# Performance work log

Hardware: AMD Instinct MI355X
Metric: run time of the kernel (lower is better)

Reference implementation:

```python
import jax, jax.numpy as jnp
import numpy as np

N_NODES = 32767   # complete binary tree, depth 15
EMB_DIM = 256
HIDDEN = 256      # 'hidden_size' -> LSTM state is 2*HIDDEN
VOCAB = 32        # len(ExprNode.TYPE_LIST)


def setup_inputs() -> dict:
    key = jax.random.key(0)
    k1, k2, k3, k4, k5, k6 = jax.random.split(key, 6)
    H2 = 2 * HIDDEN
    types = jax.random.randint(k1, (N_NODES,), 0, VOCAB, dtype=jnp.int32)
    # complete binary tree: children of node i are 2i+1 / 2i+2; sentinel slot N = zero state
    idx = np.arange(N_NODES)
    a = 2 * idx + 1
    b = 2 * idx + 2
    a = np.where(a < N_NODES, a, N_NODES).astype(np.int32)
    b = np.where(b < N_NODES, b, N_NODES).astype(np.int32)
    scale = 1.0 / np.sqrt(H2)
    return {
        "types": types,
        "a_idx": jnp.asarray(a),
        "b_idx": jnp.asarray(b),
        "emb": jax.random.normal(k2, (VOCAB, EMB_DIM), jnp.float32) * 0.02,
        "W_ih": jax.random.normal(k3, (4 * H2, EMB_DIM), jnp.float32) * scale,
        "W_hh": jax.random.normal(k4, (4 * H2, H2), jnp.float32) * scale,
        "b_ih": jax.random.normal(k5, (4 * H2,), jnp.float32) * scale,
        "b_hh": jax.random.normal(k6, (4 * H2,), jnp.float32) * scale,
    }


def reference(types, a_idx, b_idx, emb, W_ih, W_hh, b_ih, b_hh):
    """Recursive binary tree-LSTM over topological (leaves-first) order.
    Each node's LSTM state has size 2H; a parent's incoming (h, c) is the concat
    of the first H entries of each child's state (zeros for missing children).
    Returns per-node hidden outputs [N, 2H] (the out_map, indexed by node id)."""
    N = types.shape[0]
    H2 = W_hh.shape[1]
    H = H2 // 2
    # batched input projection for all nodes at once: [N, 4*H2]
    x_proj = emb[types] @ W_ih.T + (b_ih + b_hh)
    Hs0 = jnp.zeros((N + 1, H2), x_proj.dtype)  # slot N = h0 (zeros)
    Cs0 = jnp.zeros((N + 1, H2), x_proj.dtype)
    order = jnp.arange(N - 1, -1, -1)  # children (higher index) before parents

    def step(carry, i):
        Hs, Cs = carry
        h = jnp.concatenate([Hs[a_idx[i], :H], Hs[b_idx[i], :H]])  # [2H]
        c = jnp.concatenate([Cs[a_idx[i], :H], Cs[b_idx[i], :H]])
        gates = x_proj[i] + W_hh @ h                 # [4*H2], torch gate order i,f,g,o
        ig, fg, gg, og = jnp.split(gates, 4)
        c_new = jax.nn.sigmoid(fg) * c + jax.nn.sigmoid(ig) * jnp.tanh(gg)
        h_new = jax.nn.sigmoid(og) * jnp.tanh(c_new)
        return (Hs.at[i].set(h_new), Cs.at[i].set(c_new)), h_new

    _, outs = jax.lax.scan(step, (Hs0, Cs0), order)
    return outs[::-1]  # reorder so row i is node i's output
```

## Files before the change

kernel.cpp:

```cpp
#include <hip/hip_runtime.h>
#include <hip/hip_bf16.h>


#define NNODES 32767

typedef __attribute__((ext_vector_type(8))) short bf16x8;
typedef __attribute__((ext_vector_type(4))) float f32x4;

typedef const __attribute__((address_space(1))) void* gptr_t;
typedef __attribute__((address_space(3))) void* lptr_t;

__device__ __forceinline__ float sigf(float x) { return 1.0f / (1.0f + __expf(-x)); }
__device__ __forceinline__ float tanhfast(float x) { return 2.0f / (1.0f + __expf(-2.0f * x)) - 1.0f; }

__device__ __forceinline__ short bf_hi(float x) {
    __hip_bfloat16 h = __float2bfloat16(x);
    return __builtin_bit_cast(short, h);
}
__device__ __forceinline__ float bf_f(short s) {
    __hip_bfloat16 h = __builtin_bit_cast(__hip_bfloat16, s);
    return __bfloat162float(h);
}
__device__ __forceinline__ void split8(const float* src, short* hi, short* lo) {
#pragma unroll
    for (int j = 0; j < 8; ++j) {
        float x = src[j];
        short h = bf_hi(x);
        hi[j] = h;
        lo[j] = bf_hi(x - bf_f(h));
    }
}

__global__ void proj_kernel(const float* __restrict__ emb, const float* __restrict__ W_ih,
                            const float* __restrict__ b_ih, const float* __restrict__ b_hh,
                            float* __restrict__ proj) {
    __shared__ float e[256];
    int v = blockIdx.x >> 3;
    int rc = blockIdx.x & 7;
    int t = threadIdx.x;
    e[t] = emb[v * 256 + t];
    __syncthreads();
    int r = rc * 256 + t;
    const float4* w4 = (const float4*)(W_ih + (size_t)r * 256);
    const float4* e4 = (const float4*)e;
    float acc = 0.f;
#pragma unroll 8
    for (int k = 0; k < 64; ++k) {
        float4 w = w4[k];
        float4 h = e4[k];
        acc += w.x * h.x + w.y * h.y + w.z * h.z + w.w * h.w;
    }
    proj[v * 2048 + r] = acc + b_ih[r] + b_hh[r];
}

__global__ void wpack_kernel(const float* __restrict__ W_hh,
                             short* __restrict__ Whi, short* __restrict__ Wlo) {
    int t = blockIdx.x * 256 + threadIdx.x;
    int lane = t & 63;
    int kt = (t >> 6) & 15;
    int ntile = t >> 10;
    int n = ntile * 16 + (lane & 15);
    int k0 = kt * 32 + (lane >> 4) * 8;
    const float* src = W_hh + (size_t)n * 512 + k0;
    short hi[8], lo[8];
    split8(src, hi, lo);
    *(bf16x8*)(Whi + (size_t)t * 8) = *(bf16x8*)hi;
    *(bf16x8*)(Wlo + (size_t)t * 8) = *(bf16x8*)lo;
}

__global__ void leaf_kernel(const int* __restrict__ types, const float* __restrict__ proj,
                            float* __restrict__ out, float* __restrict__ C256,
                            short* __restrict__ Hsplit) {
    int bi = blockIdx.x;
    int node = 16383 + (bi >> 1);
    int j = ((bi & 1) << 8) + threadIdx.x;
    int tt = types[node];
    const float* p = proj + (size_t)tt * 2048;
    float gi = p[j];
    float gg = p[1024 + j];
    float go = p[1536 + j];
    float cn = sigf(gi) * tanhfast(gg);
    float hn = sigf(go) * tanhfast(cn);
    out[(size_t)node * 512 + j] = hn;
    if ((bi & 1) == 0) {
        C256[(size_t)node * 256 + j] = cn;
        short hi = bf_hi(hn);
        Hsplit[(size_t)node * 512 + j] = hi;
        Hsplit[(size_t)node * 512 + 256 + j] = bf_hi(hn - bf_f(hi));
    }
}

__global__ __launch_bounds__(256) void big_gemm_lstm_kernel(
    const int* __restrict__ a_idx, const int* __restrict__ b_idx,
    const int* __restrict__ types, float* __restrict__ out,
    const float* __restrict__ proj, float* __restrict__ C256,
    short* __restrict__ Hsplit, int node_base) {
    __shared__ __align__(16) short lds[2][16384];
    __shared__ int sA[128], sB[128], sT[128];

    const unsigned WOFF = 16777216u;

    int t = threadIdx.x;
    int lin = blockIdx.x;
    int x = lin >> 4;
    int y = (lin & 7) * 2 + ((lin >> 3) & 1);
    int node0 = node_base + x * 128;
    int j0 = y * 32;

    if (t < 128) {
        sA[t] = a_idx[node0 + t];
        sB[t] = b_idx[node0 + t];
        sT[t] = types[node0 + t];
    }
    __syncthreads();

    int w = t >> 6, lane = t & 63;
    int wm = w >> 1, wn = w & 1;

    unsigned b0[8], b1[8], sk;
    if (w < 2) {
        sk = 32u;
#pragma unroll
        for (int i = 0; i < 8; ++i) {
            int ca = w * 8 + i;
            int rl = lane >> 3;
            int r_loc = ca * 8 + rl;
            int j = (lane & 7) ^ rl;
            unsigned ks = (unsigned)(j >> 2) * 256u + (unsigned)(j & 3) * 8u;
            b0[i] = (unsigned)sA[r_loc] * 512u + ks;
            b1[i] = (unsigned)sB[r_loc] * 512u + ks;
        }
    } else {
        sk = 512u;
#pragma unroll
        for (int i = 0; i < 8; ++i) {
            int cc = (w - 2) * 8 + i;
            int nt = cc >> 1, part = cc & 1;
            int q = nt >> 1, sub = nt & 1;
            unsigned ntg = (unsigned)(q * 32 + y * 2 + sub);
            b0[i] = WOFF + ntg * 8192u + (unsigned)part * 1048576u + (unsigned)lane * 8u;
            b1[i] = b0[i] + 4096u;
        }
    }

    f32x4 acc[4][4];
#pragma unroll
    for (int i = 0; i < 4; ++i)
#pragma unroll
        for (int q = 0; q < 4; ++q) acc[i][q] = (f32x4){0.f, 0.f, 0.f, 0.f};

    auto stage = [&](int kt, int buf) {
#pragma unroll
        for (int i = 0; i < 8; ++i) {
            unsigned off = ((kt < 8) ? b0[i] : b1[i]) + (unsigned)(kt & 7) * sk;
            const short* gsrc = Hsplit + off;
            short* ldst = &lds[buf][(w * 8 + i) * 512];
            __builtin_amdgcn_global_load_lds((gptr_t)gsrc, (lptr_t)ldst, 16, 0, 0);
        }
    };

    auto compute = [&](int buf) {
        const short* L = lds[buf];
        int s = lane >> 4;
        bf16x8 ah[4], al[4];
#pragma unroll
        for (int i = 0; i < 4; ++i) {
            int m_loc = (wm * 4 + i) * 16 + (lane & 15);
            int ch = m_loc >> 3;
            int r = m_loc & 7;
            const short* base = L + ch * 512 + r * 64;
            ah[i] = *(const bf16x8*)&base[(s ^ r) * 8];
            al[i] = *(const bf16x8*)&base[((4 + s) ^ r) * 8];
        }
        __builtin_amdgcn_s_setprio(1);
#pragma unroll
        for (int q = 0; q < 4; ++q) {
            int nt = q * 2 + wn;
            bf16x8 bh = *(const bf16x8*)&L[(16 + nt * 2) * 512 + lane * 8];
            bf16x8 bl = *(const bf16x8*)&L[(17 + nt * 2) * 512 + lane * 8];
#pragma unroll
            for (int i = 0; i < 4; ++i) {
                acc[i][q] = __builtin_amdgcn_mfma_f32_16x16x32_bf16(ah[i], bh, acc[i][q], 0, 0, 0);
                acc[i][q] = __builtin_amdgcn_mfma_f32_16x16x32_bf16(ah[i], bl, acc[i][q], 0, 0, 0);
                acc[i][q] = __builtin_amdgcn_mfma_f32_16x16x32_bf16(al[i], bh, acc[i][q], 0, 0, 0);
            }
        }
        __builtin_amdgcn_s_setprio(0);
    };

    stage(0, 0);
    int cur = 0;
#pragma unroll 1
    for (int kt = 0; kt < 16; ++kt) {
        __builtin_amdgcn_s_barrier();
        if (kt < 15) stage(kt + 1, cur ^ 1);
        if (kt < 15) {
            asm volatile("s_waitcnt vmcnt(8)" ::: "memory");
        } else {
            asm volatile("s_waitcnt vmcnt(0)" ::: "memory");
        }
        __builtin_amdgcn_s_barrier();
        compute(cur);
        cur ^= 1;
    }

    int j = j0 + wn * 16 + (lane & 15);
    bool fh = (j < 256);
    int jc = j & 255;
#pragma unroll
    for (int i = 0; i < 4; ++i) {
        int mrow = wm * 64 + i * 16 + (lane >> 4) * 4;
#pragma unroll
        for (int r = 0; r < 4; ++r) {
            int m_loc = mrow + r;
            int node = node0 + m_loc;
            const float* p = proj + (size_t)sT[m_loc] * 2048 + j;
            float gi = acc[i][0][r] + p[0];
            float gf = acc[i][1][r] + p[512];
            float gg = acc[i][2][r] + p[1024];
            float go = acc[i][3][r] + p[1536];
            int child = fh ? sA[m_loc] : sB[m_loc];
            float c = C256[(size_t)child * 256 + jc];
            float cn = sigf(gf) * c + sigf(gi) * tanhfast(gg);
            float hn = sigf(go) * tanhfast(cn);
            out[(size_t)node * 512 + j] = hn;
            if (fh) {
                C256[(size_t)node * 256 + j] = cn;
                short hi = bf_hi(hn);
                Hsplit[(size_t)node * 512 + j] = hi;
                Hsplit[(size_t)node * 512 + 256 + j] = bf_hi(hn - bf_f(hi));
            }
        }
    }
}

__global__ __launch_bounds__(256) void gemm_lstm_kernel(
    const int* __restrict__ a_idx, const int* __restrict__ b_idx,
    const int* __restrict__ types, float* __restrict__ out,
    const short* __restrict__ Whi, const short* __restrict__ Wlo,
    const float* __restrict__ proj, float* __restrict__ C256,
    short* __restrict__ Hsplit, int node_base, int Jc) {
    __shared__ short Ahi[2][16][64][8];
    __shared__ short Alo[2][16][64][8];
    __shared__ int sA[32], sB[32], sT[32];
    int t = threadIdx.x;
    int node0 = node_base + blockIdx.x * 32;
    if (t < 32) {
        sA[t] = a_idx[node0 + t];
        sB[t] = b_idx[node0 + t];
        sT[t] = types[node0 + t];
    }
    __syncthreads();

#pragma unroll
    for (int it = 0; it < 8; ++it) {
        int c = it * 256 + t;
        int mt = c >> 10;
        int kt = (c >> 6) & 15;
        int lane = c & 63;
        int m_loc = mt * 16 + (lane & 15);
        int k0 = kt * 32 + (lane >> 4) * 8;
        int child = (k0 < 256) ? sA[m_loc] : sB[m_loc];
        const short* src = Hsplit + (size_t)child * 512 + (k0 & 255);
        *(bf16x8*)&Ahi[mt][kt][lane][0] = *(const bf16x8*)src;
        *(bf16x8*)&Alo[mt][kt][lane][0] = *(const bf16x8*)(src + 256);
    }
    __syncthreads();

    int w = t >> 6;
    int lane = t & 63;
    int jsteps = Jc >> 4;
    int jbase = blockIdx.y * Jc;

    auto epilogue = [&](int j0, f32x4 (&acc)[4][2]) {
        int j = j0 + (lane & 15);
        int jc = j & 255;
        bool fh = (j < 256);
#pragma unroll
        for (int mt = 0; mt < 2; ++mt) {
            int mrow = mt * 16 + (lane >> 4) * 4;
#pragma unroll
            for (int r = 0; r < 4; ++r) {
                int m_loc = mrow + r;
                int node = node0 + m_loc;
                const float* p = proj + (size_t)sT[m_loc] * 2048 + j;
                float gi = acc[0][mt][r] + p[0];
                float gf = acc[1][mt][r] + p[512];
                float gg = acc[2][mt][r] + p[1024];
                float go = acc[3][mt][r] + p[1536];
                int child = fh ? sA[m_loc] : sB[m_loc];
                float c = C256[(size_t)child * 256 + jc];
                float cn = sigf(gf) * c + sigf(gi) * tanhfast(gg);
                float hn = sigf(go) * tanhfast(cn);
                out[(size_t)node * 512 + j] = hn;
                if (fh) {
                    C256[(size_t)node * 256 + j] = cn;
                    short hi = bf_hi(hn);
                    Hsplit[(size_t)node * 512 + j] = hi;
                    Hsplit[(size_t)node * 512 + 256 + j] = bf_hi(hn - bf_f(hi));
                }
            }
        }
    };

    if (jsteps >= 4) {
        for (int js = w; js < jsteps; js += 4) {
            int j0 = jbase + js * 16;
            f32x4 acc[4][2];
#pragma unroll
            for (int q = 0; q < 4; ++q)
#pragma unroll
                for (int mt = 0; mt < 2; ++mt) acc[q][mt] = (f32x4){0.f, 0.f, 0.f, 0.f};
            int nt0 = j0 >> 4;
#pragma unroll 4
            for (int kt = 0; kt < 16; ++kt) {
                bf16x8 ah0 = *(const bf16x8*)&Ahi[0][kt][lane][0];
                bf16x8 al0 = *(const bf16x8*)&Alo[0][kt][lane][0];
                bf16x8 ah1 = *(const bf16x8*)&Ahi[1][kt][lane][0];
                bf16x8 al1 = *(const bf16x8*)&Alo[1][kt][lane][0];
#pragma unroll
                for (int q = 0; q < 4; ++q) {
                    int ntile = q * 32 + nt0;
                    size_t off = ((size_t)(ntile * 16 + kt) * 64 + lane) * 8;
                    bf16x8 bh = *(const bf16x8*)(Whi + off);
                    bf16x8 bl = *(const bf16x8*)(Wlo + off);
                    acc[q][0] = __builtin_amdgcn_mfma_f32_16x16x32_bf16(ah0, bh, acc[q][0], 0, 0, 0);
                    acc[q][0] = __builtin_amdgcn_mfma_f32_16x16x32_bf16(ah0, bl, acc[q][0], 0, 0, 0);
                    acc[q][0] = __builtin_amdgcn_mfma_f32_16x16x32_bf16(al0, bh, acc[q][0], 0, 0, 0);
                    acc[q][1] = __builtin_amdgcn_mfma_f32_16x16x32_bf16(ah1, bh, acc[q][1], 0, 0, 0);
                    acc[q][1] = __builtin_amdgcn_mfma_f32_16x16x32_bf16(ah1, bl, acc[q][1], 0, 0, 0);
                    acc[q][1] = __builtin_amdgcn_mfma_f32_16x16x32_bf16(al1, bh, acc[q][1], 0, 0, 0);
                }
            }
            epilogue(j0, acc);
        }
    } else {
        int js = w & 1;
        int khalf = w >> 1;
        int j0 = jbase + js * 16;
        f32x4 acc[4][2];
#pragma unroll
        for (int q = 0; q < 4; ++q)
#pragma unroll
            for (int mt = 0; mt < 2; ++mt) acc[q][mt] = (f32x4){0.f, 0.f, 0.f, 0.f};
        int nt0 = j0 >> 4;
        int kt0 = khalf * 8;
#pragma unroll 4
        for (int kt = kt0; kt < kt0 + 8; ++kt) {
            bf16x8 ah0 = *(const bf16x8*)&Ahi[0][kt][lane][0];
            bf16x8 al0 = *(const bf16x8*)&Alo[0][kt][lane][0];
            bf16x8 ah1 = *(const bf16x8*)&Ahi[1][kt][lane][0];
            bf16x8 al1 = *(const bf16x8*)&Alo[1][kt][lane][0];
#pragma unroll
            for (int q = 0; q < 4; ++q) {
                int ntile = q * 32 + nt0;
                size_t off = ((size_t)(ntile * 16 + kt) * 64 + lane) * 8;
                bf16x8 bh = *(const bf16x8*)(Whi + off);
                bf16x8 bl = *(const bf16x8*)(Wlo + off);
                acc[q][0] = __builtin_amdgcn_mfma_f32_16x16x32_bf16(ah0, bh, acc[q][0], 0, 0, 0);
                acc[q][0] = __builtin_amdgcn_mfma_f32_16x16x32_bf16(ah0, bl, acc[q][0], 0, 0, 0);
                acc[q][0] = __builtin_amdgcn_mfma_f32_16x16x32_bf16(al0, bh, acc[q][0], 0, 0, 0);
                acc[q][1] = __builtin_amdgcn_mfma_f32_16x16x32_bf16(ah1, bh, acc[q][1], 0, 0, 0);
                acc[q][1] = __builtin_amdgcn_mfma_f32_16x16x32_bf16(ah1, bl, acc[q][1], 0, 0, 0);
                acc[q][1] = __builtin_amdgcn_mfma_f32_16x16x32_bf16(al1, bh, acc[q][1], 0, 0, 0);
            }
        }
        __syncthreads();
        float* xch = (float*)&Ahi[0][0][0][0];
        if (khalf == 1) {
#pragma unroll
            for (int q = 0; q < 4; ++q)
#pragma unroll
                for (int mt = 0; mt < 2; ++mt)
                    *(f32x4*)&xch[(((q * 2 + mt) * 128) + js * 64 + lane) * 4] = acc[q][mt];
        }
        __syncthreads();
        if (khalf == 0) {
#pragma unroll
            for (int q = 0; q < 4; ++q)
#pragma unroll
                for (int mt = 0; mt < 2; ++mt) {
                    f32x4 o = *(const f32x4*)&xch[(((q * 2 + mt) * 128) + js * 64 + lane) * 4];
                    acc[q][mt] += o;
                }
            epilogue(j0, acc);
        }
    }
}

__global__ void small_gemm_kernel(
    const int* __restrict__ a_idx, const int* __restrict__ b_idx,
    const float* __restrict__ out, const float* __restrict__ W_hh,
    float* __restrict__ part, int node_base) {
    __shared__ float hs[64];
    int t = threadIdx.x;
    int n = blockIdx.x;
    int node = node_base + n;
    int kbase = blockIdx.z * 64;
    if (t < 16) {
        int child = (kbase < 256) ? a_idx[node] : b_idx[node];
        float4 v = ((const float4*)(out + (size_t)child * 512 + (kbase & 255)))[t];
        ((float4*)hs)[t] = v;
    }
    __syncthreads();
    int r = blockIdx.y * 256 + t;
    const float4* w4 = (const float4*)(W_hh + (size_t)r * 512 + kbase);
    const float4* h4 = (const float4*)hs;
    float acc = 0.f;
#pragma unroll
    for (int k = 0; k < 16; ++k) {
        float4 wv = w4[k];
        float4 hv = h4[k];
        acc += wv.x * hv.x + wv.y * hv.y + wv.z * hv.z + wv.w * hv.w;
    }
    part[((size_t)blockIdx.z * gridDim.x + n) * 2048 + r] = acc;
}

__global__ void small_combine_kernel(
    const int* __restrict__ a_idx, const int* __restrict__ b_idx,
    const int* __restrict__ types, const float* __restrict__ part,
    const float* __restrict__ proj, float* __restrict__ C256,
    short* __restrict__ Hsplit, float* __restrict__ out, int node_base, int B) {
    int bi = blockIdx.x;
    int n = bi >> 1;
    int j = ((bi & 1) << 8) + threadIdx.x;
    int node = node_base + n;
    float g[4] = {0.f, 0.f, 0.f, 0.f};
    for (int z = 0; z < 8; ++z) {
        const float* p = part + ((size_t)z * B + n) * 2048;
#pragma unroll
        for (int q = 0; q < 4; ++q) g[q] += p[q * 512 + j];
    }
    const float* p = proj + (size_t)types[node] * 2048 + j;
    float gi = g[0] + p[0];
    float gf = g[1] + p[512];
    float gg = g[2] + p[1024];
    float go = g[3] + p[1536];
    int child = (j < 256) ? a_idx[node] : b_idx[node];
    float c = C256[(size_t)child * 256 + (j & 255)];
    float cn = sigf(gf) * c + sigf(gi) * tanhfast(gg);
    float hn = sigf(go) * tanhfast(cn);
    out[(size_t)node * 512 + j] = hn;
    if (j < 256) {
        C256[(size_t)node * 256 + j] = cn;
        short hi = bf_hi(hn);
        Hsplit[(size_t)node * 512 + j] = hi;
        Hsplit[(size_t)node * 512 + 256 + j] = bf_hi(hn - bf_f(hi));
    }
}

extern "C" void kernel_launch(void* const* d_in, const int* in_sizes, int n_in,
                              void* d_out, int out_size, void* d_ws, size_t ws_size,
                              hipStream_t stream) {
    const int* types = (const int*)d_in[0];
    const int* a_idx = (const int*)d_in[1];
    const int* b_idx = (const int*)d_in[2];
    const float* emb = (const float*)d_in[3];
    const float* W_ih = (const float*)d_in[4];
    const float* W_hh = (const float*)d_in[5];
    const float* b_ih = (const float*)d_in[6];
    const float* b_hh = (const float*)d_in[7];
    float* out = (float*)d_out;

    float* ws = (float*)d_ws;
    float* proj = ws;
    float* C256 = ws + 65536;
    short* Hsplit = (short*)(C256 + 8388352);
    short* Whi = Hsplit + 16777216;
    short* Wlo = Whi + 1048576;
    float* part = (float*)(Wlo + 1048576);

    proj_kernel<<<256, 256, 0, stream>>>(emb, W_ih, b_ih, b_hh, proj);
    wpack_kernel<<<512, 256, 0, stream>>>(W_hh, Whi, Wlo);
    leaf_kernel<<<32768, 256, 0, stream>>>(types, proj, out, C256, Hsplit);

    for (int d = 13; d >= 0; --d) {
        int base = (1 << d) - 1;
        int B = 1 << d;
        if (B >= 1024) {
            int X = B / 128;
            big_gemm_lstm_kernel<<<X * 16, 256, 0, stream>>>(
                a_idx, b_idx, types, out, proj, C256, Hsplit, base);
        } else if (B >= 32) {
            int bx = B / 32;
            int J = 2;
            while (bx * J < 512 && J < 16) J <<= 1;
            gemm_lstm_kernel<<<dim3(bx, J), 256, 0, stream>>>(
                a_idx, b_idx, types, out, Whi, Wlo, proj, C256, Hsplit, base, 512 / J);
        } else {
            small_gemm_kernel<<<dim3(B, 8, 8), 256, 0, stream>>>(
                a_idx, b_idx, out, W_hh, part, base);
            small_combine_kernel<<<B * 2, 256, 0, stream>>>(
                a_idx, b_idx, types, part, proj, C256, Hsplit, out, base, B);
        }
    }
}
```

Measured before the change: 410.3 us.

## Reuse W_hh rows across all nodes in small-level GEMV via register caching

The small-level GEMM kernel used to launch one block per node, so each node re-read its slice of W_hh from fp32 global memory. It now launches a fixed 8x8 grid in which each thread loads its 64 weights once into registers, rebuilt from the packed bf16 hi/lo split, and loops over all nodes in the level. This cuts weight traffic by a factor of B for the top levels (B < 32) but gives far fewer blocks and puts 64 floats in registers per thread. The hi+lo bf16 reconstruction may differ slightly from the original fp32 weights.

```diff
diff --git a/kernel.cpp b/kernel.cpp
--- a/kernel.cpp
+++ b/kernel.cpp
@@ -388,32 +388,48 @@
     }
 }
 
-__global__ void small_gemm_kernel(
+__global__ __launch_bounds__(256) void smallv2_gemm_kernel(
     const int* __restrict__ a_idx, const int* __restrict__ b_idx,
-    const float* __restrict__ out, const float* __restrict__ W_hh,
-    float* __restrict__ part, int node_base) {
-    __shared__ float hs[64];
+    const float* __restrict__ out, const short* __restrict__ Whi,
+    float* __restrict__ part, int node_base, int B) {
+    __shared__ float hs[16][64];
+    const short* Wlo = Whi + 1048576;
+
     int t = threadIdx.x;
-    int n = blockIdx.x;
-    int node = node_base + n;
-    int kbase = blockIdx.z * 64;
-    if (t < 16) {
+    int y = blockIdx.x, z = blockIdx.y;
+    int r = y * 256 + t;
+    int kbase = z * 64;
+
+    if (t < B * 16) {
+        int n = t >> 4;
+        int f4 = t & 15;
+        int node = node_base + n;
         int child = (kbase < 256) ? a_idx[node] : b_idx[node];
-        float4 v = ((const float4*)(out + (size_t)child * 512 + (kbase & 255)))[t];
-        ((float4*)hs)[t] = v;
+        float4 v = ((const float4*)(out + (size_t)child * 512 + (kbase & 255)))[f4];
+        *(float4*)&hs[n][f4 * 4] = v;
     }
     __syncthreads();
-    int r = blockIdx.y * 256 + t;
-    const float4* w4 = (const float4*)(W_hh + (size_t)r * 512 + kbase);
-    const float4* h4 = (const float4*)hs;
-    float acc = 0.f;
-#pragma unroll
-    for (int k = 0; k < 16; ++k) {
-        float4 wv = w4[k];
-        float4 hv = h4[k];
-        acc += wv.x * hv.x + wv.y * hv.y + wv.z * hv.z + wv.w * hv.w;
-    }
-    part[((size_t)blockIdx.z * gridDim.x + n) * 2048 + r] = acc;
+
+    float wv[64];
+#pragma unroll
+    for (int u = 0; u < 8; ++u) {
+        int k = kbase + u * 8;
+        int kt = k >> 5;
+        int sub = (k >> 3) & 3;
+        size_t off = ((size_t)((r >> 4) * 16 + kt) * 64 + (sub << 4) + (r & 15)) * 8;
+        bf16x8 hi = *(const bf16x8*)(Whi + off);
+        bf16x8 lo = *(const bf16x8*)(Wlo + off);
+#pragma unroll
+        for (int e = 0; e < 8; ++e)
+            wv[u * 8 + e] = bf_f(hi[e]) + bf_f(lo[e]);
+    }
+
+    for (int n = 0; n < B; ++n) {
+        float acc = 0.f;
+#pragma unroll
+        for (int k = 0; k < 64; ++k) acc += wv[k] * hs[n][k];
+        part[((size_t)z * B + n) * 2048 + r] = acc;
+    }
 }
 
 __global__ void small_combine_kernel(
@@ -488,8 +504,8 @@
             gemm_lstm_kernel<<<dim3(bx, J), 256, 0, stream>>>(
                 a_idx, b_idx, types, out, Whi, Wlo, proj, C256, Hsplit, base, 512 / J);
         } else {
-            small_gemm_kernel<<<dim3(B, 8, 8), 256, 0, stream>>>(
-                a_idx, b_idx, out, W_hh, part, base);
+            smallv2_gemm_kernel<<<dim3(8, 8), 256, 0, stream>>>(
+                a_idx, b_idx, out, Whi, part, base, B);
             small_combine_kernel<<<B * 2, 256, 0, stream>>>(
                 a_idx, b_idx, types, part, proj, C256, Hsplit, out, base, B);
         }
```

New measurement: 402.0 us. 2.0% less time.
